# Kernel tuning notes

Measured on AMD Instinct MI355X. Metric: run time of the kernel, lower is better.

The kernel has to match this reference:

```python
import jax, jax.numpy as jnp
from jax import lax
import numpy as np

B, T, D = 16, 4096, 512          # batch, encoder length, d_model
C, FW = 10, 100                  # aconv_chans, aconv_filts (kernel width 2*FW+1)
SHARP = 2.0                      # sharpening_factor


def setup_inputs() -> dict:
    key = jax.random.key(0)
    ks = jax.random.split(key, 11)
    s = 1.0 / np.sqrt(D)
    sc = 1.0 / np.sqrt(2 * FW + 1)
    return {
        "value": jax.random.normal(ks[0], (B, T, D), jnp.float32),
        "query": jax.random.normal(ks[1], (B, D), jnp.float32),
        "input_lengths": jax.random.randint(ks[2], (B,), T // 2, T + 1),
        "att_prev": jax.random.uniform(ks[3], (B, T), jnp.float32),
        # learned parameters (torch Linear stores W as [out,in]; y = x @ W.T + b)
        "W_enc": jax.random.uniform(ks[4], (D, D), jnp.float32, -s, s),
        "b_enc": jax.random.uniform(ks[5], (D,), jnp.float32, -s, s),
        "W_dec": jax.random.uniform(ks[6], (D, D), jnp.float32, -s, s),
        "W_att": jax.random.uniform(ks[7], (D, C), jnp.float32, -s, s),
        "W_conv": jax.random.uniform(ks[8], (C, 1, 2 * FW + 1), jnp.float32, -sc, sc),
        "w_g": jax.random.uniform(ks[9], (1, D), jnp.float32, -s, s),
        "b_g": jax.random.uniform(ks[10], (1,), jnp.float32, -s, s),
    }


def reference(value, query, input_lengths, att_prev,
              W_enc, b_enc, W_dec, W_att, W_conv, w_g, b_g):
    # pre_compute_enc_h = mlp_enc(enc_h): [B,T,D]
    pre_enc = jnp.einsum('btd,ed->bte', value, W_enc) + b_enc
    # dec_z_tiled = mlp_dec(dec_z): [B,1,D]
    dec_tiled = (query @ W_dec.T)[:, None, :]
    # loc_conv: 1D conv over T, in_ch=1 -> out_ch=C, same padding -> [B,C,T]
    conv = lax.conv_general_dilated(att_prev[:, None, :], W_conv,
                                    window_strides=(1,), padding=[(FW, FW)],
                                    dimension_numbers=('NCH', 'OIH', 'NCH'))
    # mlp_att on transposed conv: [B,T,C] @ W_att.T -> [B,T,D]
    att_conv = jnp.einsum('bct,dc->btd', conv, W_att)
    # e = gvec(tanh(sum)): [B,T]
    e = jnp.einsum('btd,d->bt', jnp.tanh(att_conv + pre_enc + dec_tiled), w_g[0]) + b_g[0]
    # pad mask: positions >= length are masked to -inf (use large finite neg)
    pad_mask = jnp.arange(T)[None, :] >= input_lengths[:, None]
    e = jnp.where(pad_mask, -1e30, e)
    att_weights = jax.nn.softmax(SHARP * e, axis=1)            # [B,T]
    context = jnp.einsum('btd,bt->bd', value, att_weights)     # [B,D]
    return context, att_weights
```

## Files before the change

kernel.cpp:

```cpp
#include <hip/hip_runtime.h>
#include <hip/hip_bf16.h>

constexpr int kB  = 16;
constexpr int kT  = 4096;
constexpr int kD  = 512;
constexpr int kC  = 10;
constexpr int kFW = 100;
constexpr int kKW = 2 * kFW + 1;
constexpr int kKP = 544;

typedef __attribute__((ext_vector_type(8))) short short8_t;
typedef __attribute__((ext_vector_type(4))) float float4_t;

__device__ __forceinline__ float tanh_fast(float x) {
  float ax = fabsf(x);
  float z  = __expf(-2.0f * ax);
  float r  = (1.0f - z) / (1.0f + z);
  return copysignf(r, x);
}

__device__ __forceinline__ short f2bf(float x) {
  unsigned u = __float_as_uint(x);
  u += 0x7fffu + ((u >> 16) & 1u);
  return (short)(u >> 16);
}

__device__ __forceinline__ unsigned pk2(float lo, float hi) {
  __hip_bfloat162 h = __float22bfloat162_rn(make_float2(lo, hi));
  union { __hip_bfloat162 h2; unsigned u; } cv; cv.h2 = h; return cv.u;
}

__device__ __forceinline__ float bf2f(short s) {
  return __uint_as_float(((unsigned)(unsigned short)s) << 16);
}

__device__ __forceinline__ void glds16(const void* g, void* l) {
  __builtin_amdgcn_global_load_lds(
      (const __attribute__((address_space(1))) void*)g,
      (__attribute__((address_space(3))) void*)l, 16, 0, 0);
}

__global__ void dec_bias_kernel(const float* __restrict__ query,
                                const float* __restrict__ W_dec,
                                const float* __restrict__ b_enc,
                                float* __restrict__ bias) {
  int gw   = (blockIdx.x * blockDim.x + threadIdx.x) >> 6;
  int lane = threadIdx.x & 63;
  int b = gw >> 9;
  int d = gw & (kD - 1);
  const float* q = query + (size_t)b * kD;
  const float* w = W_dec + (size_t)d * kD;
  float s = 0.f;
#pragma unroll
  for (int k0 = 0; k0 < kD; k0 += 256) {
    float4 qa = *(const float4*)(q + k0 + lane * 4);
    float4 wa = *(const float4*)(w + k0 + lane * 4);
    s += qa.x * wa.x + qa.y * wa.y + qa.z * wa.z + qa.w * wa.w;
  }
#pragma unroll
  for (int off = 32; off > 0; off >>= 1) s += __shfl_down(s, off, 64);
  if (lane == 0) bias[gw] = b_enc[d] + s;
}

__global__ void pack_w_kernel(const float* __restrict__ W_enc,
                              const float* __restrict__ W_att,
                              short* __restrict__ Wbf) {
  int d = blockIdx.x;
  for (int c = threadIdx.x; c < kKP; c += 256) {
    float v = 0.f;
    if (c < kD)            v = W_enc[(size_t)d * kD + c];
    else if (c < kD + kC)  v = W_att[(size_t)d * kC + (c - kD)];
    Wbf[(size_t)d * kKP + c] = f2bf(v);
  }
}

__global__ void convert_kernel(const float* __restrict__ value,
                               const int* __restrict__ lens,
                               short* __restrict__ Abf) {
  int b  = blockIdx.y;
  int t0 = blockIdx.x * 64;
  if (t0 >= lens[b]) return;
  int tid = threadIdx.x;
  const float* src = value + ((size_t)b * kT + t0) * kD;
  short* dst = Abf + ((size_t)b * kT + t0) * kKP;
#pragma unroll
  for (int i = 0; i < 16; ++i) {
    int c = tid + i * 256;
    int row = c >> 6, col = (c & 63) * 8;
    float4 f0 = *(const float4*)(src + (size_t)row * kD + col);
    float4 f1 = *(const float4*)(src + (size_t)row * kD + col + 4);
    uint4 o;
    o.x = pk2(f0.x, f0.y); o.y = pk2(f0.z, f0.w);
    o.z = pk2(f1.x, f1.y); o.w = pk2(f1.z, f1.w);
    *(uint4*)(dst + (size_t)row * kKP + col) = o;
  }
}

__global__ void conv_kernel(const float* __restrict__ att_prev,
                            const float* __restrict__ W_conv,
                            short* __restrict__ Abf) {
  __shared__ float ap[256 + 2 * kFW];
  __shared__ float wc[kC * kKW];
  int b   = blockIdx.y;
  int t0  = blockIdx.x * 256;
  int tid = threadIdx.x;
  for (int i = tid; i < kC * kKW; i += 256) wc[i] = W_conv[i];
  for (int i = tid; i < 256 + 2 * kFW; i += 256) {
    int p = t0 - kFW + i;
    ap[i] = (p >= 0 && p < kT) ? att_prev[(size_t)b * kT + p] : 0.f;
  }
  __syncthreads();
  float acc[kC];
#pragma unroll
  for (int c = 0; c < kC; ++c) acc[c] = 0.f;
  for (int j = 0; j < kKW; ++j) {
    float a = ap[tid + j];
#pragma unroll
    for (int c = 0; c < kC; ++c) acc[c] += a * wc[c * kKW + j];
  }
  unsigned ow[16];
#pragma unroll
  for (int i = 0; i < 5; ++i) ow[i] = pk2(acc[2 * i], acc[2 * i + 1]);
#pragma unroll
  for (int i = 5; i < 16; ++i) ow[i] = 0u;
  uint4* out = (uint4*)(Abf + ((size_t)b * kT + t0 + tid) * kKP + kD);
  out[0] = make_uint4(ow[0], ow[1], ow[2], ow[3]);
  out[1] = make_uint4(ow[4], ow[5], ow[6], ow[7]);
  out[2] = make_uint4(ow[8], ow[9], ow[10], ow[11]);
  out[3] = make_uint4(ow[12], ow[13], ow[14], ow[15]);
}

constexpr int BM = 128, BN = 128, BK = 32;

__global__ __launch_bounds__(256) void e_kernel(
    const short* __restrict__ Abf, const short* __restrict__ Wbf,
    const float* __restrict__ bias, const float* __restrict__ w_g,
    const int* __restrict__ lens, float* __restrict__ e_part) {
  __shared__ short As[BM * BK];
  __shared__ short Bs[BN * BK];

  int tid = threadIdx.x;
  int L    = blockIdx.x;
  int xcd  = L & 7;
  int slot = L >> 3;
  int bn   = slot & 3;
  int mt   = xcd * 64 + (slot >> 2);
  int b  = mt >> 5;
  int t0 = (mt & 31) * BM;
  if (t0 >= lens[b]) return;
  int n0 = bn * BN;

  int w    = tid >> 6;
  int lane = tid & 63;
  int nl   = lane & 15;
  int quad = lane >> 4;
  int wm = w >> 1, wn = w & 1;

  int kps = (lane & 3) ^ ((lane >> 3) & 3);
  const short* asrc0 = Abf + ((size_t)(b * kT + t0) + w * 32 + (lane >> 2)) * kKP + kps * 8;
  const short* asrc1 = asrc0 + (size_t)16 * kKP;
  short* adst0 = &As[(w * 32) * BK];
  short* adst1 = &As[(w * 32 + 16) * BK];
  const short* bsrc0 = Wbf + (size_t)(n0 + w * 32 + (lane >> 2)) * kKP + kps * 8;
  const short* bsrc1 = bsrc0 + (size_t)16 * kKP;
  short* bdst0 = &Bs[(w * 32) * BK];
  short* bdst1 = &Bs[(w * 32 + 16) * BK];

  int swz = quad ^ ((nl >> 1) & 3);
  const short8_t* ard = (const short8_t*)&As[(((wm * 64 + nl) << 2) + swz) * 8];
  const short8_t* brd = (const short8_t*)&Bs[(((wn * 64 + nl) << 2) + swz) * 8];

  float4_t acc[4][4] = {};

  for (int kk = 0; kk < 17; ++kk) {
    int ko = kk * BK;
    __syncthreads();
    glds16(asrc0 + ko, adst0);
    glds16(asrc1 + ko, adst1);
    glds16(bsrc0 + ko, bdst0);
    glds16(bsrc1 + ko, bdst1);
    __syncthreads();
    short8_t a_frag[4], b_frag[4];
#pragma unroll
    for (int i = 0; i < 4; ++i) a_frag[i] = ard[i * 64];
#pragma unroll
    for (int j = 0; j < 4; ++j) b_frag[j] = brd[j * 64];
#pragma unroll
    for (int i = 0; i < 4; ++i)
#pragma unroll
      for (int j = 0; j < 4; ++j)
        acc[i][j] = __builtin_amdgcn_mfma_f32_16x16x32_bf16(
            a_frag[i], b_frag[j], acc[i][j], 0, 0, 0);
  }

  float bias_r[4], wg_r[4];
#pragma unroll
  for (int j = 0; j < 4; ++j) {
    int d = n0 + wn * 64 + j * 16 + nl;
    bias_r[j] = bias[b * kD + d];
    wg_r[j]   = w_g[d];
  }
  int p = wn * 4 + bn;
  float* ep = e_part + ((size_t)p * kB + b) * kT + t0 + wm * 64;
#pragma unroll
  for (int i = 0; i < 4; ++i) {
#pragma unroll
    for (int r = 0; r < 4; ++r) {
      float s = 0.f;
#pragma unroll
      for (int j = 0; j < 4; ++j)
        s += wg_r[j] * tanh_fast(acc[i][j][r] + bias_r[j]);
      s += __shfl_xor(s, 1, 64);
      s += __shfl_xor(s, 2, 64);
      s += __shfl_xor(s, 4, 64);
      s += __shfl_xor(s, 8, 64);
      if (nl == 0) ep[i * 16 + quad * 4 + r] = s;
    }
  }
}

__global__ void softmax_kernel(const float* __restrict__ e_part,
                               const int* __restrict__ lens,
                               float* __restrict__ att) {
  __shared__ float eb[kT];
  __shared__ float sred[256];
  int b = blockIdx.x, tid = threadIdx.x;
  int len = lens[b];
  const float* ep = e_part + (size_t)b * kT;
  float m = -3.0e38f;
  for (int t = tid; t < len; t += 256) {
    float s = 0.f;
#pragma unroll
    for (int p = 0; p < 8; ++p) s += ep[(size_t)p * kB * kT + t];
    eb[t] = s;
    m = fmaxf(m, s);
  }
  sred[tid] = m; __syncthreads();
  for (int s = 128; s > 0; s >>= 1) {
    if (tid < s) sred[tid] = fmaxf(sred[tid], sred[tid + s]);
    __syncthreads();
  }
  m = sred[0]; __syncthreads();
  float sum = 0.f;
  for (int t = tid; t < len; t += 256) sum += __expf(2.0f * (eb[t] - m));
  sred[tid] = sum; __syncthreads();
  for (int s = 128; s > 0; s >>= 1) {
    if (tid < s) sred[tid] += sred[tid + s];
    __syncthreads();
  }
  float inv = 1.0f / sred[0];
  for (int t = tid; t < kT; t += 256)
    att[(size_t)b * kT + t] = (t < len) ? __expf(2.0f * (eb[t] - m)) * inv : 0.0f;
}

__global__ void context_kernel(const short* __restrict__ Abf,
                               const float* __restrict__ att,
                               const int* __restrict__ lens,
                               float* __restrict__ ctx) {
  __shared__ float red[4][kD];
  int b = blockIdx.y;
  int len = lens[b];
  int t0 = blockIdx.x * 128;
  if (t0 >= len) return;
  int w = threadIdx.x >> 6, lane = threadIdx.x & 63;
  int tb = t0 + w * 32;
  int tmax = min(32, len - tb);
  float a[8] = {0.f, 0.f, 0.f, 0.f, 0.f, 0.f, 0.f, 0.f};
  const short* vp = Abf + ((size_t)b * kT + tb) * kKP + lane * 8;
  const float* ap = att + (size_t)b * kT + tb;
  for (int t = 0; t < tmax; ++t) {
    float wt = ap[t];
    short8_t v = *(const short8_t*)(vp + (size_t)t * kKP);
#pragma unroll
    for (int i = 0; i < 8; ++i) a[i] += wt * bf2f(v[i]);
  }
#pragma unroll
  for (int i = 0; i < 8; ++i) red[w][lane * 8 + i] = a[i];
  __syncthreads();
  int tid = threadIdx.x;
  for (int col = tid; col < kD; col += 256) {
    float s = red[0][col] + red[1][col] + red[2][col] + red[3][col];
    atomicAdd(&ctx[b * kD + col], s);
  }
}

extern "C" void kernel_launch(void* const* d_in, const int* in_sizes, int n_in,
                              void* d_out, int out_size, void* d_ws, size_t ws_size,
                              hipStream_t stream) {
  const float* value    = (const float*)d_in[0];
  const float* query    = (const float*)d_in[1];
  const int*   lens     = (const int*)  d_in[2];
  const float* att_prev = (const float*)d_in[3];
  const float* W_enc    = (const float*)d_in[4];
  const float* b_enc    = (const float*)d_in[5];
  const float* W_dec    = (const float*)d_in[6];
  const float* W_att    = (const float*)d_in[7];
  const float* W_conv   = (const float*)d_in[8];
  const float* w_g      = (const float*)d_in[9];

  float* ws     = (float*)d_ws;
  float* e_part = ws;
  float* bias   = e_part + (size_t)8 * kB * kT;
  short* Wbf    = (short*)(bias + (size_t)kB * kD);
  short* Abf    = Wbf + (size_t)kD * kKP;
  float* ctx = (float*)d_out;
  float* att = ctx + (size_t)kB * kD;

  hipMemsetAsync(ctx, 0, (size_t)kB * kD * sizeof(float), stream);

  dec_bias_kernel<<<kB * kD / 4, 256, 0, stream>>>(query, W_dec, b_enc, bias);
  pack_w_kernel<<<kD, 256, 0, stream>>>(W_enc, W_att, Wbf);
  convert_kernel<<<dim3(kT / 64, kB), 256, 0, stream>>>(value, lens, Abf);
  conv_kernel<<<dim3(kT / 256, kB), 256, 0, stream>>>(att_prev, W_conv, Abf);
  e_kernel<<<2048, 256, 0, stream>>>(Abf, Wbf, bias, w_g, lens, e_part);
  softmax_kernel<<<kB, 256, 0, stream>>>(e_part, lens, att);
  context_kernel<<<dim3(kT / 128, kB), 256, 0, stream>>>(Abf, att, lens, ctx);
}
```

Before: 325.5 us.

## Fuse prep kernels, widen GEMM K-tile to 64, split softmax into chunked passes

Merges the four preprocessing kernels into a single launch that dispatches on block index, which removes launch overhead. The padded K stride grows to 576 so the e_kernel can use 64-wide K tiles with a new XOR swizzle, giving 9 iterations instead of 17 and fewer barriers. The M-tile to XCD mapping is interleaved differently. The single-block-per-batch softmax becomes a two-pass chunked softmax that runs on more blocks, and the memset of ctx is folded into the second pass. In exchange the padding traffic is larger and there is an extra launch plus workspace round-trips for eb and stats.

Result: faster. 295.6 us (-9.2%).

```diff
diff --git a/kernel.cpp b/kernel.cpp
--- a/kernel.cpp
+++ b/kernel.cpp
@@ -7,7 +7,7 @@
 constexpr int kC  = 10;
 constexpr int kFW = 100;
 constexpr int kKW = 2 * kFW + 1;
-constexpr int kKP = 544;
+constexpr int kKP = 576;
 
 typedef __attribute__((ext_vector_type(8))) short short8_t;
 typedef __attribute__((ext_vector_type(4))) float float4_t;
@@ -40,115 +40,106 @@
       (__attribute__((address_space(3))) void*)l, 16, 0, 0);
 }
 
-__global__ void dec_bias_kernel(const float* __restrict__ query,
-                                const float* __restrict__ W_dec,
-                                const float* __restrict__ b_enc,
-                                float* __restrict__ bias) {
-  int gw   = (blockIdx.x * blockDim.x + threadIdx.x) >> 6;
-  int lane = threadIdx.x & 63;
-  int b = gw >> 9;
-  int d = gw & (kD - 1);
-  const float* q = query + (size_t)b * kD;
-  const float* w = W_dec + (size_t)d * kD;
-  float s = 0.f;
-#pragma unroll
-  for (int k0 = 0; k0 < kD; k0 += 256) {
-    float4 qa = *(const float4*)(q + k0 + lane * 4);
-    float4 wa = *(const float4*)(w + k0 + lane * 4);
-    s += qa.x * wa.x + qa.y * wa.y + qa.z * wa.z + qa.w * wa.w;
-  }
-#pragma unroll
-  for (int off = 32; off > 0; off >>= 1) s += __shfl_down(s, off, 64);
-  if (lane == 0) bias[gw] = b_enc[d] + s;
-}
-
-__global__ void pack_w_kernel(const float* __restrict__ W_enc,
-                              const float* __restrict__ W_att,
-                              short* __restrict__ Wbf) {
-  int d = blockIdx.x;
-  for (int c = threadIdx.x; c < kKP; c += 256) {
-    float v = 0.f;
-    if (c < kD)            v = W_enc[(size_t)d * kD + c];
-    else if (c < kD + kC)  v = W_att[(size_t)d * kC + (c - kD)];
-    Wbf[(size_t)d * kKP + c] = f2bf(v);
-  }
-}
-
-__global__ void convert_kernel(const float* __restrict__ value,
-                               const int* __restrict__ lens,
-                               short* __restrict__ Abf) {
-  int b  = blockIdx.y;
-  int t0 = blockIdx.x * 64;
-  if (t0 >= lens[b]) return;
-  int tid = threadIdx.x;
-  const float* src = value + ((size_t)b * kT + t0) * kD;
-  short* dst = Abf + ((size_t)b * kT + t0) * kKP;
-#pragma unroll
-  for (int i = 0; i < 16; ++i) {
-    int c = tid + i * 256;
-    int row = c >> 6, col = (c & 63) * 8;
-    float4 f0 = *(const float4*)(src + (size_t)row * kD + col);
-    float4 f1 = *(const float4*)(src + (size_t)row * kD + col + 4);
-    uint4 o;
-    o.x = pk2(f0.x, f0.y); o.y = pk2(f0.z, f0.w);
-    o.z = pk2(f1.x, f1.y); o.w = pk2(f1.z, f1.w);
-    *(uint4*)(dst + (size_t)row * kKP + col) = o;
-  }
-}
-
-__global__ void conv_kernel(const float* __restrict__ att_prev,
-                            const float* __restrict__ W_conv,
-                            short* __restrict__ Abf) {
+__global__ __launch_bounds__(256) void prep_kernel(
+    const float* __restrict__ query, const float* __restrict__ W_dec,
+    const float* __restrict__ b_enc, float* __restrict__ bias,
+    const float* __restrict__ W_enc, const float* __restrict__ W_att,
+    short* __restrict__ Wbf,
+    const float* __restrict__ att_prev, const float* __restrict__ W_conv,
+    const float* __restrict__ value, const int* __restrict__ lens,
+    short* __restrict__ Abf) {
   __shared__ float ap[256 + 2 * kFW];
   __shared__ float wc[kC * kKW];
-  int b   = blockIdx.y;
-  int t0  = blockIdx.x * 256;
+  int blk = blockIdx.x;
   int tid = threadIdx.x;
-  for (int i = tid; i < kC * kKW; i += 256) wc[i] = W_conv[i];
-  for (int i = tid; i < 256 + 2 * kFW; i += 256) {
-    int p = t0 - kFW + i;
-    ap[i] = (p >= 0 && p < kT) ? att_prev[(size_t)b * kT + p] : 0.f;
-  }
-  __syncthreads();
-  float acc[kC];
-#pragma unroll
-  for (int c = 0; c < kC; ++c) acc[c] = 0.f;
-  for (int j = 0; j < kKW; ++j) {
-    float a = ap[tid + j];
-#pragma unroll
-    for (int c = 0; c < kC; ++c) acc[c] += a * wc[c * kKW + j];
-  }
-  unsigned ow[16];
-#pragma unroll
-  for (int i = 0; i < 5; ++i) ow[i] = pk2(acc[2 * i], acc[2 * i + 1]);
-#pragma unroll
-  for (int i = 5; i < 16; ++i) ow[i] = 0u;
-  uint4* out = (uint4*)(Abf + ((size_t)b * kT + t0 + tid) * kKP + kD);
-  out[0] = make_uint4(ow[0], ow[1], ow[2], ow[3]);
-  out[1] = make_uint4(ow[4], ow[5], ow[6], ow[7]);
-  out[2] = make_uint4(ow[8], ow[9], ow[10], ow[11]);
-  out[3] = make_uint4(ow[12], ow[13], ow[14], ow[15]);
-}
-
-constexpr int BM = 128, BN = 128, BK = 32;
+
+  if (blk < 2048) {
+    int gw   = (blk * 256 + tid) >> 6;
+    int lane = tid & 63;
+    int b = gw >> 9, d = gw & (kD - 1);
+    const float* q = query + (size_t)b * kD;
+    const float* w = W_dec + (size_t)d * kD;
+    float s = 0.f;
+#pragma unroll
+    for (int k0 = 0; k0 < kD; k0 += 256) {
+      float4 qa = *(const float4*)(q + k0 + lane * 4);
+      float4 wa = *(const float4*)(w + k0 + lane * 4);
+      s += qa.x * wa.x + qa.y * wa.y + qa.z * wa.z + qa.w * wa.w;
+    }
+#pragma unroll
+    for (int off = 32; off > 0; off >>= 1) s += __shfl_down(s, off, 64);
+    if (lane == 0) bias[gw] = b_enc[d] + s;
+  } else if (blk < 2048 + 512) {
+    int d = blk - 2048;
+    for (int c = tid; c < kKP; c += 256) {
+      float v = 0.f;
+      if (c < kD)           v = W_enc[(size_t)d * kD + c];
+      else if (c < kD + kC) v = W_att[(size_t)d * kC + (c - kD)];
+      Wbf[(size_t)d * kKP + c] = f2bf(v);
+    }
+  } else if (blk < 2048 + 512 + 256) {
+    int lin = blk - 2560;
+    int b = lin >> 4, t0 = (lin & 15) * 256;
+    for (int i = tid; i < kC * kKW; i += 256) wc[i] = W_conv[i];
+    for (int i = tid; i < 256 + 2 * kFW; i += 256) {
+      int p = t0 - kFW + i;
+      ap[i] = (p >= 0 && p < kT) ? att_prev[(size_t)b * kT + p] : 0.f;
+    }
+    __syncthreads();
+    float acc[kC];
+#pragma unroll
+    for (int c = 0; c < kC; ++c) acc[c] = 0.f;
+    for (int j = 0; j < kKW; ++j) {
+      float a = ap[tid + j];
+#pragma unroll
+      for (int c = 0; c < kC; ++c) acc[c] += a * wc[c * kKW + j];
+    }
+    unsigned ow[32];
+#pragma unroll
+    for (int i = 0; i < 5; ++i) ow[i] = pk2(acc[2 * i], acc[2 * i + 1]);
+#pragma unroll
+    for (int i = 5; i < 32; ++i) ow[i] = 0u;
+    uint4* out = (uint4*)(Abf + ((size_t)b * kT + t0 + tid) * kKP + kD);
+#pragma unroll
+    for (int i = 0; i < 8; ++i)
+      out[i] = make_uint4(ow[4 * i], ow[4 * i + 1], ow[4 * i + 2], ow[4 * i + 3]);
+  } else {
+    int lin = blk - 2816;
+    int b = lin >> 6, t0 = (lin & 63) * 64;
+    if (t0 >= lens[b]) return;
+    const float* src = value + ((size_t)b * kT + t0) * kD;
+    short* dst = Abf + ((size_t)b * kT + t0) * kKP;
+#pragma unroll
+    for (int i = 0; i < 16; ++i) {
+      int c = tid + i * 256;
+      int row = c >> 6, col = (c & 63) * 8;
+      float4 f0 = *(const float4*)(src + (size_t)row * kD + col);
+      float4 f1 = *(const float4*)(src + (size_t)row * kD + col + 4);
+      uint4 o;
+      o.x = pk2(f0.x, f0.y); o.y = pk2(f0.z, f0.w);
+      o.z = pk2(f1.x, f1.y); o.w = pk2(f1.z, f1.w);
+      *(uint4*)(dst + (size_t)row * kKP + col) = o;
+    }
+  }
+}
 
 __global__ __launch_bounds__(256) void e_kernel(
     const short* __restrict__ Abf, const short* __restrict__ Wbf,
     const float* __restrict__ bias, const float* __restrict__ w_g,
     const int* __restrict__ lens, float* __restrict__ e_part) {
-  __shared__ short As[BM * BK];
-  __shared__ short Bs[BN * BK];
+  __shared__ short As[128 * 64];
+  __shared__ short Bs[128 * 64];
 
   int tid = threadIdx.x;
   int L    = blockIdx.x;
   int xcd  = L & 7;
   int slot = L >> 3;
   int bn   = slot & 3;
-  int mt   = xcd * 64 + (slot >> 2);
+  int mt   = (slot >> 2) * 8 + xcd;
   int b  = mt >> 5;
-  int t0 = (mt & 31) * BM;
+  int t0 = (mt & 31) * 128;
   if (t0 >= lens[b]) return;
-  int n0 = bn * BN;
+  int n0 = bn * 128;
 
   int w    = tid >> 6;
   int lane = tid & 63;
@@ -156,41 +147,45 @@
   int quad = lane >> 4;
   int wm = w >> 1, wn = w & 1;
 
-  int kps = (lane & 3) ^ ((lane >> 3) & 3);
-  const short* asrc0 = Abf + ((size_t)(b * kT + t0) + w * 32 + (lane >> 2)) * kKP + kps * 8;
-  const short* asrc1 = asrc0 + (size_t)16 * kKP;
-  short* adst0 = &As[(w * 32) * BK];
-  short* adst1 = &As[(w * 32 + 16) * BK];
-  const short* bsrc0 = Wbf + (size_t)(n0 + w * 32 + (lane >> 2)) * kKP + kps * 8;
-  const short* bsrc1 = bsrc0 + (size_t)16 * kKP;
-  short* bdst0 = &Bs[(w * 32) * BK];
-  short* bdst1 = &Bs[(w * 32 + 16) * BK];
-
-  int swz = quad ^ ((nl >> 1) & 3);
-  const short8_t* ard = (const short8_t*)&As[(((wm * 64 + nl) << 2) + swz) * 8];
-  const short8_t* brd = (const short8_t*)&Bs[(((wn * 64 + nl) << 2) + swz) * 8];
+  int r8 = lane >> 3;
+  int kc = (lane & 7) ^ r8;
+  const short* asrc = Abf + ((size_t)(b * kT + t0) + w * 32 + r8) * kKP + kc * 8;
+  const short* bsrc = Wbf + (size_t)(n0 + w * 32 + r8) * kKP + kc * 8;
+  short* adst = &As[(w * 32) * 64];
+  short* bdst = &Bs[(w * 32) * 64];
+
+  int axr = nl & 7;
+  const short* aBase = &As[(wm * 64 + nl) * 64];
+  const short* bBase = &Bs[(wn * 64 + nl) * 64];
+  int co0 = ((0 * 4 + quad) ^ axr) * 8;
+  int co1 = ((1 * 4 + quad) ^ axr) * 8;
 
   float4_t acc[4][4] = {};
 
-  for (int kk = 0; kk < 17; ++kk) {
-    int ko = kk * BK;
-    __syncthreads();
-    glds16(asrc0 + ko, adst0);
-    glds16(asrc1 + ko, adst1);
-    glds16(bsrc0 + ko, bdst0);
-    glds16(bsrc1 + ko, bdst1);
-    __syncthreads();
-    short8_t a_frag[4], b_frag[4];
-#pragma unroll
-    for (int i = 0; i < 4; ++i) a_frag[i] = ard[i * 64];
-#pragma unroll
-    for (int j = 0; j < 4; ++j) b_frag[j] = brd[j * 64];
-#pragma unroll
-    for (int i = 0; i < 4; ++i)
-#pragma unroll
-      for (int j = 0; j < 4; ++j)
-        acc[i][j] = __builtin_amdgcn_mfma_f32_16x16x32_bf16(
-            a_frag[i], b_frag[j], acc[i][j], 0, 0, 0);
+  for (int kk = 0; kk < 9; ++kk) {
+    int ko = kk * 64;
+    __syncthreads();
+#pragma unroll
+    for (int j = 0; j < 4; ++j) {
+      glds16(asrc + ko + (size_t)(j * 8) * kKP, adst + j * 8 * 64);
+      glds16(bsrc + ko + (size_t)(j * 8) * kKP, bdst + j * 8 * 64);
+    }
+    __syncthreads();
+#pragma unroll
+    for (int ks = 0; ks < 2; ++ks) {
+      int co = ks ? co1 : co0;
+      short8_t a_frag[4], b_frag[4];
+#pragma unroll
+      for (int i = 0; i < 4; ++i) a_frag[i] = *(const short8_t*)(aBase + i * 1024 + co);
+#pragma unroll
+      for (int j = 0; j < 4; ++j) b_frag[j] = *(const short8_t*)(bBase + j * 1024 + co);
+#pragma unroll
+      for (int i = 0; i < 4; ++i)
+#pragma unroll
+        for (int j = 0; j < 4; ++j)
+          acc[i][j] = __builtin_amdgcn_mfma_f32_16x16x32_bf16(
+              a_frag[i], b_frag[j], acc[i][j], 0, 0, 0);
+    }
   }
 
   float bias_r[4], wg_r[4];
@@ -219,21 +214,31 @@
   }
 }
 
-__global__ void softmax_kernel(const float* __restrict__ e_part,
-                               const int* __restrict__ lens,
-                               float* __restrict__ att) {
-  __shared__ float eb[kT];
+__global__ void softmax1_kernel(const float* __restrict__ e_part,
+                                const int* __restrict__ lens,
+                                float* __restrict__ eb,
+                                float* __restrict__ stats) {
   __shared__ float sred[256];
-  int b = blockIdx.x, tid = threadIdx.x;
+  int b = blockIdx.x >> 3, ch = blockIdx.x & 7;
+  int tid = threadIdx.x;
   int len = lens[b];
-  const float* ep = e_part + (size_t)b * kT;
+  int base = ch * 512;
+  const float* ep = e_part + (size_t)b * kT + base;
+  float v[2];
   float m = -3.0e38f;
-  for (int t = tid; t < len; t += 256) {
-    float s = 0.f;
-#pragma unroll
-    for (int p = 0; p < 8; ++p) s += ep[(size_t)p * kB * kT + t];
-    eb[t] = s;
-    m = fmaxf(m, s);
+#pragma unroll
+  for (int i = 0; i < 2; ++i) {
+    int t = tid + i * 256;
+    if (base + t < len) {
+      float s = 0.f;
+#pragma unroll
+      for (int p = 0; p < 8; ++p) s += ep[(size_t)p * kB * kT + t];
+      eb[(size_t)b * kT + base + t] = s;
+      v[i] = s;
+      m = fmaxf(m, s);
+    } else {
+      v[i] = -3.0e38f;
+    }
   }
   sred[tid] = m; __syncthreads();
   for (int s = 128; s > 0; s >>= 1) {
@@ -241,16 +246,47 @@
     __syncthreads();
   }
   m = sred[0]; __syncthreads();
-  float sum = 0.f;
-  for (int t = tid; t < len; t += 256) sum += __expf(2.0f * (eb[t] - m));
-  sred[tid] = sum; __syncthreads();
+  float l = 0.f;
+#pragma unroll
+  for (int i = 0; i < 2; ++i)
+    if (v[i] > -1.0e38f) l += __expf(2.0f * (v[i] - m));
+  sred[tid] = l; __syncthreads();
   for (int s = 128; s > 0; s >>= 1) {
     if (tid < s) sred[tid] += sred[tid + s];
     __syncthreads();
   }
-  float inv = 1.0f / sred[0];
-  for (int t = tid; t < kT; t += 256)
-    att[(size_t)b * kT + t] = (t < len) ? __expf(2.0f * (eb[t] - m)) * inv : 0.0f;
+  if (tid == 0) {
+    stats[(b * 8 + ch) * 2]     = m;
+    stats[(b * 8 + ch) * 2 + 1] = sred[0];
+  }
+}
+
+__global__ void softmax2_kernel(const float* __restrict__ eb,
+                                const float* __restrict__ stats,
+                                const int* __restrict__ lens,
+                                float* __restrict__ att,
+                                float* __restrict__ ctx) {
+  int b = blockIdx.x, tid = threadIdx.x;
+  int len = lens[b];
+  ctx[b * kD + tid * 2]     = 0.f;
+  ctx[b * kD + tid * 2 + 1] = 0.f;
+  float M = -3.0e38f;
+#pragma unroll
+  for (int p = 0; p < 8; ++p) M = fmaxf(M, stats[(b * 8 + p) * 2]);
+  float L = 0.f;
+#pragma unroll
+  for (int p = 0; p < 8; ++p) {
+    float mc = stats[(b * 8 + p) * 2], lc = stats[(b * 8 + p) * 2 + 1];
+    if (lc > 0.f) L += lc * __expf(2.0f * (mc - M));
+  }
+  float inv = 1.0f / L;
+  const float* e = eb + (size_t)b * kT;
+  float* a = att + (size_t)b * kT;
+#pragma unroll
+  for (int i = 0; i < 16; ++i) {
+    int t = tid + i * 256;
+    a[t] = (t < len) ? __expf(2.0f * (e[t] - M)) * inv : 0.0f;
+  }
 }
 
 __global__ void context_kernel(const short* __restrict__ Abf,
@@ -300,19 +336,19 @@
 
   float* ws     = (float*)d_ws;
   float* e_part = ws;
-  float* bias   = e_part + (size_t)8 * kB * kT;
+  float* eb     = e_part + (size_t)8 * kB * kT;
+  float* stats  = eb + (size_t)kB * kT;
+  float* bias   = stats + 256;
   short* Wbf    = (short*)(bias + (size_t)kB * kD);
   short* Abf    = Wbf + (size_t)kD * kKP;
   float* ctx = (float*)d_out;
   float* att = ctx + (size_t)kB * kD;
 
-  hipMemsetAsync(ctx, 0, (size_t)kB * kD * sizeof(float), stream);
-
-  dec_bias_kernel<<<kB * kD / 4, 256, 0, stream>>>(query, W_dec, b_enc, bias);
-  pack_w_kernel<<<kD, 256, 0, stream>>>(W_enc, W_att, Wbf);
-  convert_kernel<<<dim3(kT / 64, kB), 256, 0, stream>>>(value, lens, Abf);
-  conv_kernel<<<dim3(kT / 256, kB), 256, 0, stream>>>(att_prev, W_conv, Abf);
+  prep_kernel<<<3840, 256, 0, stream>>>(query, W_dec, b_enc, bias,
+                                        W_enc, W_att, Wbf,
+                                        att_prev, W_conv, value, lens, Abf);
   e_kernel<<<2048, 256, 0, stream>>>(Abf, Wbf, bias, w_g, lens, e_part);
-  softmax_kernel<<<kB, 256, 0, stream>>>(e_part, lens, att);
+  softmax1_kernel<<<kB * 8, 256, 0, stream>>>(e_part, lens, eb, stats);
+  softmax2_kernel<<<kB, 256, 0, stream>>>(eb, stats, lens, att, (float*)d_out);
   context_kernel<<<dim3(kT / 128, kB), 256, 0, stream>>>(Abf, att, lens, ctx);
 }
```
